# Optimization experiments

Measured on AMD Instinct MI355X. Metric: run time of the kernel, lower is better.

Reference implementation:

```python
import jax, jax.numpy as jnp
import numpy as np

# cfg dims: B batch, LQ max_que_len, O max_opt_count, LO max_opt_len,
# S max_sent_para, W max_words_sent, D word_emb
B, LQ, O, LO, S, W, D = 64, 64, 8, 32, 64, 32, 512
NEG_BIG = -9.0e15  # torch masked_fill constant for empty sentences


def setup_inputs() -> dict:
    key = jax.random.key(0)
    k1, k2, k3 = jax.random.split(key, 3)
    que_feat = jax.random.normal(k1, (B, LQ, D), dtype=jnp.float32)
    opt_feat = jax.random.normal(k2, (B, O, LO, D), dtype=jnp.float32)
    csf = jax.random.normal(k3, (B, S, W, D), dtype=jnp.float32)
    csf_mask = jnp.zeros((B, S, W), dtype=bool)   # True = padding word
    opt_sum = jnp.zeros((B, O), dtype=bool)       # True = empty option
    return dict(que_feat=que_feat, opt_feat=opt_feat, csf=csf,
                csf_mask=csf_mask, opt_sum=opt_sum)


def reference(que_feat, opt_feat, csf, csf_mask, opt_sum):
    b, s, w, d = csf.shape
    o = opt_feat.shape[1]

    # per-sentence valid length; empty sentences get a huge-magnitude divisor
    csf_len = jnp.sum(~csf_mask, axis=-1)                      # [B,S]
    csf_len = jnp.where(csf_len == 0, NEG_BIG,
                        csf_len.astype(jnp.float32))

    # question -> context sentence score: sum over query words and sentence
    # words of dot products (original: matmul + two sums, fused here)
    att_q2c = jnp.einsum('bqd,bswd->bs', que_feat, csf)        # [B,S]
    ix_q2c = jnp.argmax(att_q2c / csf_len, axis=-1)            # [B]

    # gather best sentence per batch item, broadcast over options
    que_csf = jnp.take_along_axis(
        csf, ix_q2c[:, None, None, None], axis=1)[:, 0]        # [B,W,D]
    que_csf = jnp.broadcast_to(que_csf[:, None], (b, o, w, d))
    que_csf = jnp.where(opt_sum[:, :, None, None], 0.0, que_csf)

    # option -> context sentence score
    att_o2c = jnp.einsum('bold,bswd->bos', opt_feat, csf)      # [B,O,S]
    ix_o2c = jnp.argmax(att_o2c / csf_len[:, None, :], axis=-1)  # [B,O]

    # faithful to original get_opt2csf: indexes csf[0] for EVERY batch item
    opt_csf = csf[0][ix_o2c]                                   # [B,O,W,D]
    opt_csf = jnp.where(opt_sum[:, :, None, None], 0.0, opt_csf)

    # make_mask: positions whose feature vector is all-zero
    que_csf_mask = jnp.sum(jnp.abs(que_csf), axis=-1) == 0     # [B,O,W]
    opt_csf_mask = jnp.sum(jnp.abs(opt_csf), axis=-1) == 0     # [B,O,W]
    return que_csf, que_csf_mask, opt_csf, opt_csf_mask
```

## Files before the change

kernel.cpp:

```cpp
#include <hip/hip_runtime.h>
#include <stddef.h>

#define B  64
#define LQ 64
#define O  8
#define LO 32
#define S  64
#define W  32
#define D  512

#define NEG_BIG (-9.0e15f)

#define QUE_CSF_SZ  (B*O*W*D)
#define MASK_SZ     (B*O*W)
#define OFF_QMASK   (QUE_CSF_SZ)
#define OFF_OPT     (QUE_CSF_SZ + MASK_SZ)
#define OFF_OMASK   (QUE_CSF_SZ + MASK_SZ + QUE_CSF_SZ)

#define WS_QSUM 0
#define WS_OSUM (B*D)
#define WS_SC   (B*D + B*O*D)

using f4 = __attribute__((ext_vector_type(4))) float;

__device__ inline float dot4(f4 a, f4 b) {
  return a.x * b.x + a.y * b.y + a.z * b.z + a.w * b.w;
}

#define RED(v)                \
  do {                        \
    v += __shfl_xor(v, 32);   \
    v += __shfl_xor(v, 16);   \
    v += __shfl_xor(v, 8);    \
    v += __shfl_xor(v, 4);    \
    v += __shfl_xor(v, 2);    \
    v += __shfl_xor(v, 1);    \
  } while (0)

template <int ROWS>
__device__ inline void rowsum4(const f4* __restrict__ src, f4* __restrict__ dst,
                               int t) {
  const int quarter = t >> 7;
  const int col = t & 127;
  const f4* p = src + (size_t)(quarter * (ROWS / 4)) * (D / 4) + col;
  f4 acc = {0.f, 0.f, 0.f, 0.f};
  #pragma unroll
  for (int r = 0; r < ROWS / 4; ++r)
    acc += p[(size_t)r * (D / 4)];
  __shared__ f4 tmp[3][128];
  if (quarter) tmp[quarter - 1][col] = acc;
  __syncthreads();
  if (quarter == 0) dst[col] = acc + tmp[0][col] + tmp[1][col] + tmp[2][col];
}

__global__ __launch_bounds__(512) void k_qosum(
    const float* __restrict__ que, const float* __restrict__ opt,
    float* __restrict__ ws) {
  const int blk = blockIdx.x;
  const int t = threadIdx.x;
  if (blk < B) {
    rowsum4<LQ>((const f4*)(que + (size_t)blk * LQ * D),
                (f4*)(ws + WS_QSUM + (size_t)blk * D), t);
  } else {
    const int bo = blk - B;
    rowsum4<LO>((const f4*)(opt + (size_t)bo * LO * D),
                (f4*)(ws + WS_OSUM + (size_t)bo * D), t);
  }
}

__global__ __launch_bounds__(128) void k_score(
    const float* __restrict__ csf, const unsigned char* __restrict__ csf_mask,
    float* __restrict__ ws) {
  const int bs = blockIdx.x;
  const int b = bs >> 6;
  const int s = bs & 63;
  const int t = threadIdx.x;
  const int wv = t >> 6;
  const int lane = t & 63;

  const f4* src = (const f4*)(csf + (size_t)bs * W * D) + t;
  f4 acc = {0.f, 0.f, 0.f, 0.f};
  #pragma unroll 16
  for (int r = 0; r < W; ++r)
    acc += src[(size_t)r * (D / 4)];

  float pq = dot4(acc, ((const f4*)(ws + WS_QSUM + (size_t)b * D))[t]);
  float po[O];
  #pragma unroll
  for (int o = 0; o < O; ++o)
    po[o] = dot4(acc, ((const f4*)(ws + WS_OSUM + ((size_t)b * O + o) * D))[t]);

  RED(pq);
  #pragma unroll
  for (int o = 0; o < O; ++o) RED(po[o]);

  __shared__ float part[2][9];
  if (lane == 0) {
    part[wv][0] = pq;
    #pragma unroll
    for (int o = 0; o < O; ++o) part[wv][1 + o] = po[o];
  }

  int pad = 0;
  if (lane < W) pad = (csf_mask[(size_t)bs * W + lane] != 0) ? 1 : 0;
  const unsigned long long bal = __ballot(pad);
  const int valid = W - (int)__popcll(bal);
  const float len = (valid == 0) ? NEG_BIG : (float)valid;

  __syncthreads();
  if (t < 9)
    ws[WS_SC + ((size_t)t * B + b) * S + s] = (part[0][t] + part[1][t]) / len;
}

__global__ __launch_bounds__(128) void k_gather(
    const float* __restrict__ csf, const unsigned char* __restrict__ opt_sum,
    const float* __restrict__ ws, float* __restrict__ out) {
  const int bow = blockIdx.x;
  const int w = bow & 31;
  const int bo = bow >> 5;
  const int b = bo >> 3;
  const int o = bo & 7;
  const int t = threadIdx.x;
  const int wv = t >> 6;
  const int lane = t & 63;

  __shared__ int sh_ix[2];
  {
    const int q = (wv == 0) ? 0 : (1 + o);
    float v = ws[WS_SC + ((size_t)q * B + b) * S + lane];
    int idx = lane;
    for (int off = 32; off; off >>= 1) {
      float ov = __shfl_xor(v, off);
      int oi = __shfl_xor(idx, off);
      if (ov > v || (ov == v && oi < idx)) { v = ov; idx = oi; }
    }
    if (lane == 0) sh_ix[wv] = idx;
  }
  __syncthreads();

  const bool zero = (opt_sum[bo] != 0);
  f4 vq = {0.f, 0.f, 0.f, 0.f};
  f4 vo = {0.f, 0.f, 0.f, 0.f};
  if (!zero) {
    const int iq = sh_ix[0];
    const int io = sh_ix[1];
    vq = ((const f4*)(csf + (((size_t)b * S + iq) * W + w) * D))[t];
    vo = ((const f4*)(csf + (((size_t)io) * W + w) * D))[t];
  }
  __builtin_nontemporal_store(vq, (f4*)(out + (size_t)bow * D) + t);
  __builtin_nontemporal_store(vo, (f4*)(out + OFF_OPT + (size_t)bow * D) + t);

  float aq = fabsf(vq.x) + fabsf(vq.y) + fabsf(vq.z) + fabsf(vq.w);
  float ao = fabsf(vo.x) + fabsf(vo.y) + fabsf(vo.z) + fabsf(vo.w);
  for (int off = 32; off; off >>= 1) {
    aq += __shfl_xor(aq, off);
    ao += __shfl_xor(ao, off);
  }

  __shared__ float sq[2], so[2];
  if (lane == 0) { sq[wv] = aq; so[wv] = ao; }
  __syncthreads();
  if (t == 0) {
    out[OFF_QMASK + bow] = ((sq[0] + sq[1]) == 0.f) ? 1.f : 0.f;
    out[OFF_OMASK + bow] = ((so[0] + so[1]) == 0.f) ? 1.f : 0.f;
  }
}

extern "C" void kernel_launch(void* const* d_in, const int* in_sizes, int n_in,
                              void* d_out, int out_size, void* d_ws, size_t ws_size,
                              hipStream_t stream) {
  const float* que = (const float*)d_in[0];
  const float* opt = (const float*)d_in[1];
  const float* csf = (const float*)d_in[2];
  const unsigned char* csf_mask = (const unsigned char*)d_in[3];
  const unsigned char* opt_sum = (const unsigned char*)d_in[4];
  float* out = (float*)d_out;
  float* ws = (float*)d_ws;

  k_qosum<<<B + B * O, 512, 0, stream>>>(que, opt, ws);

  k_score<<<B * S, 128, 0, stream>>>(csf, csf_mask, ws);

  k_gather<<<B * O * W, 128, 0, stream>>>(csf, opt_sum, ws, out);
}
```

Before: 71.92 us.

## Fuse question/option row sums and sentence scoring into one cooperative grid kernel

Replaces the separate row-sum and scoring kernels with a single cooperative kernel of 2368 blocks. Each block streams one or two csf sentences plus, for some blocks, a half of a question or one option, then uses a grid-wide sync before the dot products. This removes a kernel boundary and overlaps the que/opt reductions with the csf streaming. It adds per-call host queries (device properties, occupancy) and a grid barrier. It relies on all 2368 blocks being co-resident, and falls back to the old two-kernel path otherwise.

```diff
diff --git a/kernel.cpp b/kernel.cpp
--- a/kernel.cpp
+++ b/kernel.cpp
@@ -1,5 +1,8 @@
 #include <hip/hip_runtime.h>
+#include <hip/hip_cooperative_groups.h>
 #include <stddef.h>
+
+namespace cg = cooperative_groups;
 
 #define B  64
 #define LQ 64
@@ -17,9 +20,11 @@
 #define OFF_OPT     (QUE_CSF_SZ + MASK_SZ)
 #define OFF_OMASK   (QUE_CSF_SZ + MASK_SZ + QUE_CSF_SZ)
 
-#define WS_QSUM 0
-#define WS_OSUM (B*D)
-#define WS_SC   (B*D + B*O*D)
+#define WS_QSUMH 0
+#define WS_OSUM  (B*2*D)
+#define WS_SC    (B*2*D + B*O*D)
+
+#define NBLK 2368
 
 using f4 = __attribute__((ext_vector_type(4))) float;
 
@@ -37,16 +42,100 @@
     v += __shfl_xor(v, 1);    \
   } while (0)
 
+__device__ inline f4 stream32(const f4* __restrict__ p, int t) {
+  f4 acc = {0.f, 0.f, 0.f, 0.f};
+  #pragma unroll 8
+  for (int r = 0; r < 32; ++r) acc += p[(size_t)r * 128 + t];
+  return acc;
+}
+
+__device__ inline void dots9(const float* __restrict__ ws, f4 acc, int b,
+                             int wv, int lane, float part[2][9]) {
+  const f4* qh = (const f4*)(ws + WS_QSUMH) + (size_t)b * 256;
+  const int t = wv * 64 + lane;
+  f4 qs = qh[t] + qh[128 + t];
+  float pq = dot4(acc, qs);
+  float po[O];
+  #pragma unroll
+  for (int o = 0; o < O; ++o)
+    po[o] = dot4(acc, ((const f4*)(ws + WS_OSUM))[((size_t)(b * O + o)) * 128 + t]);
+  RED(pq);
+  #pragma unroll
+  for (int o = 0; o < O; ++o) RED(po[o]);
+  if (lane == 0) {
+    part[wv][0] = pq;
+    #pragma unroll
+    for (int o = 0; o < O; ++o) part[wv][1 + o] = po[o];
+  }
+}
+
+__global__ __launch_bounds__(128, 5) void k_fused(
+    const float* __restrict__ que, const float* __restrict__ opt,
+    const float* __restrict__ csf, const unsigned char* __restrict__ csf_mask,
+    float* __restrict__ ws) {
+  const int blk = blockIdx.x;
+  const int t = threadIdx.x;
+  const int wv = t >> 6;
+  const int lane = t & 63;
+  const int g1 = blk + NBLK;
+  const bool j1csf = (g1 < 4096);
+
+  f4 acc0 = stream32((const f4*)csf + (size_t)blk * 4096, t);
+  f4 acc1;
+  if (j1csf) {
+    acc1 = stream32((const f4*)csf + (size_t)g1 * 4096, t);
+  } else if (g1 < 4224) {
+    const int idx = g1 - 4096;
+    const int b = idx >> 1, h = idx & 1;
+    acc1 = stream32((const f4*)que + ((size_t)b * LQ + h * 32) * 128, t);
+    ((f4*)(ws + WS_QSUMH))[(size_t)idx * 128 + t] = acc1;
+  } else {
+    const int bo = g1 - 4224;
+    acc1 = stream32((const f4*)opt + (size_t)bo * LO * 128, t);
+    ((f4*)(ws + WS_OSUM))[(size_t)bo * 128 + t] = acc1;
+  }
+
+  __threadfence();
+  cg::this_grid().sync();
+
+  __shared__ float part[2][2][9];
+  dots9(ws, acc0, blk >> 6, wv, lane, part[0]);
+  if (j1csf) dots9(ws, acc1, g1 >> 6, wv, lane, part[1]);
+
+  float len;
+  {
+    const int bs = (wv == 0) ? blk : g1;
+    int pad = 0;
+    if (lane < W && (wv == 0 || j1csf))
+      pad = (csf_mask[(size_t)bs * W + lane] != 0) ? 1 : 0;
+    const unsigned long long bal = __ballot(pad);
+    const int valid = W - (int)__popcll(bal);
+    len = (valid == 0) ? NEG_BIG : (float)valid;
+  }
+  __syncthreads();
+
+  if (t < 9) {
+    const int b0 = blk >> 6, s0 = blk & 63;
+    ws[WS_SC + ((size_t)t * B + b0) * S + s0] =
+        (part[0][0][t] + part[0][1][t]) / len;
+  }
+  if (j1csf && t >= 64 && t < 73) {
+    const int q = t - 64;
+    const int b1 = g1 >> 6, s1 = g1 & 63;
+    ws[WS_SC + ((size_t)q * B + b1) * S + s1] =
+        (part[1][0][q] + part[1][1][q]) / len;
+  }
+}
+
 template <int ROWS>
 __device__ inline void rowsum4(const f4* __restrict__ src, f4* __restrict__ dst,
                                int t) {
   const int quarter = t >> 7;
   const int col = t & 127;
-  const f4* p = src + (size_t)(quarter * (ROWS / 4)) * (D / 4) + col;
+  const f4* p = src + (size_t)(quarter * (ROWS / 4)) * 128 + col;
   f4 acc = {0.f, 0.f, 0.f, 0.f};
   #pragma unroll
-  for (int r = 0; r < ROWS / 4; ++r)
-    acc += p[(size_t)r * (D / 4)];
+  for (int r = 0; r < ROWS / 4; ++r) acc += p[(size_t)r * 128];
   __shared__ f4 tmp[3][128];
   if (quarter) tmp[quarter - 1][col] = acc;
   __syncthreads();
@@ -59,12 +148,16 @@
   const int blk = blockIdx.x;
   const int t = threadIdx.x;
   if (blk < B) {
-    rowsum4<LQ>((const f4*)(que + (size_t)blk * LQ * D),
-                (f4*)(ws + WS_QSUM + (size_t)blk * D), t);
+    rowsum4<LQ>((const f4*)que + (size_t)blk * LQ * 128,
+                (f4*)(ws + WS_QSUMH) + (size_t)blk * 256, t);
+    if (t < 128) {
+      f4 z = {0.f, 0.f, 0.f, 0.f};
+      ((f4*)(ws + WS_QSUMH))[(size_t)blk * 256 + 128 + t] = z;
+    }
   } else {
     const int bo = blk - B;
-    rowsum4<LO>((const f4*)(opt + (size_t)bo * LO * D),
-                (f4*)(ws + WS_OSUM + (size_t)bo * D), t);
+    rowsum4<LO>((const f4*)opt + (size_t)bo * LO * 128,
+                (f4*)(ws + WS_OSUM) + (size_t)bo * 128, t);
   }
 }
 
@@ -78,28 +171,10 @@
   const int wv = t >> 6;
   const int lane = t & 63;
 
-  const f4* src = (const f4*)(csf + (size_t)bs * W * D) + t;
-  f4 acc = {0.f, 0.f, 0.f, 0.f};
-  #pragma unroll 16
-  for (int r = 0; r < W; ++r)
-    acc += src[(size_t)r * (D / 4)];
-
-  float pq = dot4(acc, ((const f4*)(ws + WS_QSUM + (size_t)b * D))[t]);
-  float po[O];
-  #pragma unroll
-  for (int o = 0; o < O; ++o)
-    po[o] = dot4(acc, ((const f4*)(ws + WS_OSUM + ((size_t)b * O + o) * D))[t]);
-
-  RED(pq);
-  #pragma unroll
-  for (int o = 0; o < O; ++o) RED(po[o]);
+  f4 acc = stream32((const f4*)csf + (size_t)bs * 4096, t);
 
   __shared__ float part[2][9];
-  if (lane == 0) {
-    part[wv][0] = pq;
-    #pragma unroll
-    for (int o = 0; o < O; ++o) part[wv][1 + o] = po[o];
-  }
+  dots9(ws, acc, b, wv, lane, part);
 
   int pad = 0;
   if (lane < W) pad = (csf_mask[(size_t)bs * W + lane] != 0) ? 1 : 0;
@@ -144,8 +219,8 @@
   if (!zero) {
     const int iq = sh_ix[0];
     const int io = sh_ix[1];
-    vq = ((const f4*)(csf + (((size_t)b * S + iq) * W + w) * D))[t];
-    vo = ((const f4*)(csf + (((size_t)io) * W + w) * D))[t];
+    vq = ((const f4*)csf)[(((size_t)b * S + iq) * W + w) * 128 + t];
+    vo = ((const f4*)csf)[((size_t)io * W + w) * 128 + t];
   }
   __builtin_nontemporal_store(vq, (f4*)(out + (size_t)bow * D) + t);
   __builtin_nontemporal_store(vo, (f4*)(out + OFF_OPT + (size_t)bow * D) + t);
@@ -177,9 +252,32 @@
   float* out = (float*)d_out;
   float* ws = (float*)d_ws;
 
-  k_qosum<<<B + B * O, 512, 0, stream>>>(que, opt, ws);
-
-  k_score<<<B * S, 128, 0, stream>>>(csf, csf_mask, ws);
+  int coop = 0;
+  {
+    int dev = 0;
+    hipDeviceProp_t prop{};
+    int mb = 0;
+    if (hipGetDevice(&dev) == hipSuccess &&
+        hipGetDeviceProperties(&prop, dev) == hipSuccess &&
+        hipOccupancyMaxActiveBlocksPerMultiprocessor(&mb, k_fused, 128, 0) ==
+            hipSuccess) {
+      if (prop.cooperativeLaunch &&
+          (long)mb * prop.multiProcessorCount >= NBLK)
+        coop = 1;
+    }
+  }
+
+  if (coop) {
+    void* args[] = {(void*)&que, (void*)&opt, (void*)&csf, (void*)&csf_mask,
+                    (void*)&ws};
+    if (hipLaunchCooperativeKernel(k_fused, dim3(NBLK), dim3(128), args, 0,
+                                   stream) != hipSuccess)
+      coop = 0;
+  }
+  if (!coop) {
+    k_qosum<<<B + B * O, 512, 0, stream>>>(que, opt, ws);
+    k_score<<<B * S, 128, 0, stream>>>(csf, csf_mask, ws);
+  }
 
   k_gather<<<B * O * W, 128, 0, stream>>>(csf, opt_sum, ws, out);
 }
```

New measurement: 70.63 us. Within noise of the previous version (-1.8%).
